# Kernel optimization log

Hardware: AMD Instinct MI355X
Metric: run time of the kernel (lower is better)

The kernel has to match this reference:

```python
import jax, jax.numpy as jnp
import numpy as np


def setup_inputs() -> dict:
    key = jax.random.key(0)
    k1, k2 = jax.random.split(key)
    B, H, W, D, K = 32, 64, 64, 64, 512
    inputs = jax.random.normal(k1, (B, H, W, D), dtype=jnp.float32)
    # codebook: (D, K) as in the keras layer (embedding_dim x num_embeddings)
    embeddings = jax.random.uniform(k2, (D, K), dtype=jnp.float32,
                                    minval=-1.0, maxval=1.0) * (3.0 / D) ** 0.5
    return {"inputs": inputs, "embeddings": embeddings}


def reference(inputs, embeddings):
    # inputs: [B, H, W, D]; embeddings: [D, K]
    D = inputs.shape[-1]
    flat = inputs.reshape(-1, D)                                   # [N, D]
    distances = (jnp.sum(flat * flat, axis=1, keepdims=True)
                 - 2.0 * (flat @ embeddings)
                 + jnp.sum(embeddings * embeddings, axis=0, keepdims=True))
    encoding_indices = jnp.argmin(distances, axis=1)               # [N]
    encoding_indices = encoding_indices.reshape(inputs.shape[:-1])  # [B, H, W]
    quantized = jnp.take(embeddings.T, encoding_indices, axis=0)   # [B, H, W, D]
    # straight-through estimator
    return inputs + jax.lax.stop_gradient(quantized - inputs)
```

## Files before the change

kernel.cpp:

```cpp
#include <hip/hip_runtime.h>


#define KC 512
#define DD 64
#define TAU 5e-4f
#define HTAU (0.5f * TAU)

typedef __attribute__((ext_vector_type(8))) short short8;
typedef __attribute__((ext_vector_type(4))) float float4v;

__device__ inline unsigned short f2bf(float f) {
    unsigned u = __float_as_uint(f);
    return (unsigned short)((u + 0x7FFF + ((u >> 16) & 1)) >> 16);
}
__device__ inline float bf2f(unsigned short b) {
    return __uint_as_float((unsigned)b << 16);
}

__global__ __launch_bounds__(256) void vq_prep(const float* __restrict__ emb,
                                               float* __restrict__ et,
                                               float* __restrict__ bias,
                                               short* __restrict__ Bh,
                                               short* __restrict__ Bl) {
    __shared__ float tile[DD][17];
    const int ct = blockIdx.x;
    const int t  = threadIdx.x;

    {
        const int d = t >> 2, c0 = (t & 3) * 4;
        float4 v = *(const float4*)(emb + (size_t)d * KC + ct * 16 + c0);
        tile[d][c0 + 0] = v.x; tile[d][c0 + 1] = v.y;
        tile[d][c0 + 2] = v.z; tile[d][c0 + 3] = v.w;
    }
    __syncthreads();

    if (t < 16) {
        float s = 0.f;
        #pragma unroll
        for (int d = 0; d < DD; ++d) { float v = tile[d][t]; s += v * v; }
        bias[ct * 16 + t] = s;
    }

    {
        const int c = t >> 4, d0 = (t & 15) * 4;
        float4 v;
        v.x = tile[d0 + 0][c]; v.y = tile[d0 + 1][c];
        v.z = tile[d0 + 2][c]; v.w = tile[d0 + 3][c];
        *(float4*)(et + (size_t)(ct * 16 + c) * DD + d0) = v;
    }

    {
        const int term = t >> 7;
        const int kc   = (t >> 6) & 1;
        const int l    = t & 63;
        const int c    = l & 15, dq = l >> 4;
        short v8[8];
        #pragma unroll
        for (int j = 0; j < 8; ++j) {
            float f = tile[kc * 32 + dq * 8 + j][c];
            unsigned short h = f2bf(f);
            v8[j] = (short)(term == 0 ? h : f2bf(f - bf2f(h)));
        }
        short* dst = (term == 0 ? Bh : Bl) + ((size_t)(ct * 2 + kc) * 64 + l) * 8;
        *(short8*)dst = *(short8*)v8;
    }
}

__global__ __launch_bounds__(512, 4) void vq_main(const float* __restrict__ x_in,
                                                  const short* __restrict__ Bh,
                                                  const short* __restrict__ Bl,
                                                  const float* __restrict__ bias,
                                                  const float* __restrict__ et,
                                                  float* __restrict__ out) {
    __shared__ __align__(16) short Bh_lds[16 * 2 * 64 * 8];
    __shared__ __align__(16) short Bl_lds[16 * 2 * 64 * 8];
    __shared__ float bias_s[KC];
    __shared__ int   k1s[8][32];
    __shared__ float gaps[8][32];

    const int t = threadIdx.x, w = t >> 6, l = t & 63;
    const int col = l & 15, quad = l >> 4;
    const int R0 = blockIdx.x * 256;
    const int wrow0 = w * 32;

    {
        const float4* srcH = (const float4*)Bh;
        const float4* srcL = (const float4*)Bl;
        float4* dstH = (float4*)Bh_lds;
        float4* dstL = (float4*)Bl_lds;
        #pragma unroll
        for (int j = 0; j < 4; ++j) {
            const int idx = t + j * 512;
            dstH[idx] = srcH[idx];
            dstL[idx] = srcL[idx];
        }
        bias_s[t] = bias[t];
    }

    short8 AH[2][2], AL[2][2];
    #pragma unroll
    for (int rt = 0; rt < 2; ++rt)
        #pragma unroll
        for (int kc = 0; kc < 2; ++kc) {
            const float* p = x_in + (size_t)(R0 + wrow0 + rt * 16 + col) * DD
                           + kc * 32 + quad * 8;
            float4 xa = *(const float4*)p;
            float4 xb = *(const float4*)(p + 4);
            float f[8] = {xa.x, xa.y, xa.z, xa.w, xb.x, xb.y, xb.z, xb.w};
            short8 hi8, lo8;
            #pragma unroll
            for (int j = 0; j < 8; ++j) {
                unsigned short h = f2bf(f[j]);
                hi8[j] = (short)h;
                lo8[j] = (short)f2bf(f[j] - bf2f(h));
            }
            AH[rt][kc] = hi8;
            AL[rt][kc] = lo8;
        }
    __syncthreads();

    float m1[2][4], m2[2][4];
    int   kb[2][4];
    #pragma unroll
    for (int rt = 0; rt < 2; ++rt)
        #pragma unroll
        for (int r = 0; r < 4; ++r) {
            m1[rt][r] = -3.4e38f; m2[rt][r] = -3.4e38f; kb[rt][r] = 0;
        }

    #pragma unroll 1
    for (int h = 0; h < 2; ++h) {
        if (h == 1) {
            __syncthreads();
            const float4* srcH = (const float4*)Bh + 2048;
            const float4* srcL = (const float4*)Bl + 2048;
            float4* dstH = (float4*)Bh_lds;
            float4* dstL = (float4*)Bl_lds;
            #pragma unroll
            for (int j = 0; j < 4; ++j) {
                const int idx = t + j * 512;
                dstH[idx] = srcH[idx];
                dstL[idx] = srcL[idx];
            }
            __syncthreads();
        }

        #pragma unroll 2
        for (int ctl = 0; ctl < 16; ++ctl) {
            short8 bh0 = *(const short8*)&Bh_lds[((ctl * 2 + 0) * 64 + l) * 8];
            short8 bh1 = *(const short8*)&Bh_lds[((ctl * 2 + 1) * 64 + l) * 8];
            short8 bl0 = *(const short8*)&Bl_lds[((ctl * 2 + 0) * 64 + l) * 8];
            short8 bl1 = *(const short8*)&Bl_lds[((ctl * 2 + 1) * 64 + l) * 8];
            const int kk = h * 256 + ctl * 16 + col;
            const float ci = -0.5f * bias_s[kk];
            #pragma unroll
            for (int rt = 0; rt < 2; ++rt) {
                float4v c = {ci, ci, ci, ci};
                c = __builtin_amdgcn_mfma_f32_16x16x32_bf16(AH[rt][0], bh0, c, 0, 0, 0);
                c = __builtin_amdgcn_mfma_f32_16x16x32_bf16(AH[rt][1], bh1, c, 0, 0, 0);
                c = __builtin_amdgcn_mfma_f32_16x16x32_bf16(AL[rt][0], bh0, c, 0, 0, 0);
                c = __builtin_amdgcn_mfma_f32_16x16x32_bf16(AL[rt][1], bh1, c, 0, 0, 0);
                c = __builtin_amdgcn_mfma_f32_16x16x32_bf16(AH[rt][0], bl0, c, 0, 0, 0);
                c = __builtin_amdgcn_mfma_f32_16x16x32_bf16(AH[rt][1], bl1, c, 0, 0, 0);
                #pragma unroll
                for (int r = 0; r < 4; ++r) {
                    float cr = c[r];
                    bool gt = cr > m1[rt][r];
                    m2[rt][r] = fmaxf(fminf(cr, m1[rt][r]), m2[rt][r]);
                    kb[rt][r] = gt ? kk : kb[rt][r];
                    m1[rt][r] = fmaxf(m1[rt][r], cr);
                }
            }
        }
    }

    #pragma unroll
    for (int rt = 0; rt < 2; ++rt)
        #pragma unroll
        for (int r = 0; r < 4; ++r) {
            float b1 = m1[rt][r], b2 = m2[rt][r];
            int   bk = kb[rt][r];
            #pragma unroll
            for (int m = 1; m <= 8; m <<= 1) {
                float o1 = __shfl_xor(b1, m, 64);
                float o2 = __shfl_xor(b2, m, 64);
                int   ok = __shfl_xor(bk, m, 64);
                float n2 = fmaxf(fmaxf(b2, o2), fminf(b1, o1));
                bool take = (o1 > b1) || (o1 == b1 && ok < bk);
                b1 = take ? o1 : b1;
                bk = take ? ok : bk;
                b2 = n2;
            }
            if (col == 0) {
                const int rowl = rt * 16 + quad * 4 + r;
                k1s[w][rowl]  = bk;
                gaps[w][rowl] = b1 - b2;
            }
        }

    {
        unsigned long long mask = __ballot((l < 32) && (gaps[w][l & 31] <= HTAU));
        mask &= 0xFFFFFFFFull;
        while (mask) {
            const int rr = __builtin_ctzll(mask);
            mask &= mask - 1;
            const size_t grow = (size_t)(R0 + wrow0 + rr) * DD;
            const int kbase = l * 8;
            float acc[8];
            #pragma unroll
            for (int j = 0; j < 8; ++j) acc[j] = 0.f;
            for (int d0 = 0; d0 < DD; d0 += 4) {
                float4 xv = *(const float4*)(x_in + grow + d0);
                #pragma unroll
                for (int j = 0; j < 8; ++j) {
                    float4 ev = *(const float4*)(et + (size_t)(kbase + j) * DD + d0);
                    acc[j] += xv.x * ev.x;
                    acc[j] += xv.y * ev.y;
                    acc[j] += xv.z * ev.z;
                    acc[j] += xv.w * ev.w;
                }
            }
            float4 b0 = *(const float4*)(bias + kbase);
            float4 b1v = *(const float4*)(bias + kbase + 4);
            float bb[8] = {b0.x, b0.y, b0.z, b0.w, b1v.x, b1v.y, b1v.z, b1v.w};
            float bv = 3.4e38f; int bk = 0;
            #pragma unroll
            for (int j = 0; j < 8; ++j) {
                float s = bb[j] - 2.f * acc[j];
                if (s < bv) { bv = s; bk = kbase + j; }
            }
            #pragma unroll
            for (int m = 1; m <= 32; m <<= 1) {
                float ov = __shfl_xor(bv, m, 64);
                int   ok = __shfl_xor(bk, m, 64);
                if (ov < bv || (ov == bv && ok < bk)) { bv = ov; bk = ok; }
            }
            if (l == 0) k1s[w][rr] = bk;
        }
    }

    {
        const int c4 = col * 4;
        #pragma unroll
        for (int i = 0; i < 8; ++i) {
            const int rowl = i * 4 + quad;
            const int bk = k1s[w][rowl];
            float4 v = *(const float4*)(et + (size_t)bk * DD + c4);
            *(float4*)(out + (size_t)(R0 + wrow0 + rowl) * DD + c4) = v;
        }
    }
}

extern "C" void kernel_launch(void* const* d_in, const int* in_sizes, int n_in,
                              void* d_out, int out_size, void* d_ws, size_t ws_size,
                              hipStream_t stream) {
    const float* x_in = (const float*)d_in[0];
    const float* emb  = (const float*)d_in[1];
    float* out = (float*)d_out;

    float* et   = (float*)d_ws;
    float* bias = et + KC * DD;
    short* Bh   = (short*)(bias + KC);
    short* Bl   = Bh + 32 * 2 * 64 * 8;

    const int N = out_size / DD;

    vq_prep<<<32, 256, 0, stream>>>(emb, et, bias, Bh, Bl);
    vq_main<<<N / 256, 512, 0, stream>>>(x_in, Bh, Bl, bias, et, out);
}
```

Baseline: 119.9 us.

## Double-buffer codebook tiles in LDS with async global-to-LDS loads

Result: no change. 119.5 us (-0.4%).

```diff
diff --git a/kernel.cpp b/kernel.cpp
--- a/kernel.cpp
+++ b/kernel.cpp
@@ -15,6 +15,12 @@
 }
 __device__ inline float bf2f(unsigned short b) {
     return __uint_as_float((unsigned)b << 16);
+}
+
+__device__ inline void gload16(const void* gsrc, void* ldst) {
+    __builtin_amdgcn_global_load_lds(
+        (const __attribute__((address_space(1))) void*)gsrc,
+        (__attribute__((address_space(3))) void*)ldst, 16, 0, 0);
 }
 
 __global__ __launch_bounds__(256) void vq_prep(const float* __restrict__ emb,
@@ -72,8 +78,8 @@
                                                   const float* __restrict__ bias,
                                                   const float* __restrict__ et,
                                                   float* __restrict__ out) {
-    __shared__ __align__(16) short Bh_lds[16 * 2 * 64 * 8];
-    __shared__ __align__(16) short Bl_lds[16 * 2 * 64 * 8];
+    __shared__ __align__(16) short Bh_lds[2][8 * 2 * 64 * 8];
+    __shared__ __align__(16) short Bl_lds[2][8 * 2 * 64 * 8];
     __shared__ float bias_s[KC];
     __shared__ int   k1s[8][32];
     __shared__ float gaps[8][32];
@@ -86,13 +92,11 @@
     {
         const float4* srcH = (const float4*)Bh;
         const float4* srcL = (const float4*)Bl;
-        float4* dstH = (float4*)Bh_lds;
-        float4* dstL = (float4*)Bl_lds;
-        #pragma unroll
-        for (int j = 0; j < 4; ++j) {
+        #pragma unroll
+        for (int j = 0; j < 2; ++j) {
             const int idx = t + j * 512;
-            dstH[idx] = srcH[idx];
-            dstL[idx] = srcL[idx];
+            gload16(srcH + idx, &Bh_lds[0][idx * 8]);
+            gload16(srcL + idx, &Bl_lds[0][idx * 8]);
         }
         bias_s[t] = bias[t];
     }
@@ -129,29 +133,31 @@
         }
 
     #pragma unroll 1
-    for (int h = 0; h < 2; ++h) {
-        if (h == 1) {
-            __syncthreads();
-            const float4* srcH = (const float4*)Bh + 2048;
-            const float4* srcL = (const float4*)Bl + 2048;
-            float4* dstH = (float4*)Bh_lds;
-            float4* dstL = (float4*)Bl_lds;
-            #pragma unroll
-            for (int j = 0; j < 4; ++j) {
+    for (int st = 0; st < 4; ++st) {
+        const int cur = st & 1;
+
+        if (st < 3) {
+            const float4* srcH = (const float4*)Bh + (st + 1) * 1024;
+            const float4* srcL = (const float4*)Bl + (st + 1) * 1024;
+            short* dH = Bh_lds[cur ^ 1];
+            short* dL = Bl_lds[cur ^ 1];
+            #pragma unroll
+            for (int j = 0; j < 2; ++j) {
                 const int idx = t + j * 512;
-                dstH[idx] = srcH[idx];
-                dstL[idx] = srcL[idx];
-            }
-            __syncthreads();
-        }
-
+                gload16(srcH + idx, dH + idx * 8);
+                gload16(srcL + idx, dL + idx * 8);
+            }
+        }
+
+        const short* BhS = Bh_lds[cur];
+        const short* BlS = Bl_lds[cur];
         #pragma unroll 2
-        for (int ctl = 0; ctl < 16; ++ctl) {
-            short8 bh0 = *(const short8*)&Bh_lds[((ctl * 2 + 0) * 64 + l) * 8];
-            short8 bh1 = *(const short8*)&Bh_lds[((ctl * 2 + 1) * 64 + l) * 8];
-            short8 bl0 = *(const short8*)&Bl_lds[((ctl * 2 + 0) * 64 + l) * 8];
-            short8 bl1 = *(const short8*)&Bl_lds[((ctl * 2 + 1) * 64 + l) * 8];
-            const int kk = h * 256 + ctl * 16 + col;
+        for (int ctl = 0; ctl < 8; ++ctl) {
+            short8 bh0 = *(const short8*)&BhS[((ctl * 2 + 0) * 64 + l) * 8];
+            short8 bh1 = *(const short8*)&BhS[((ctl * 2 + 1) * 64 + l) * 8];
+            short8 bl0 = *(const short8*)&BlS[((ctl * 2 + 0) * 64 + l) * 8];
+            short8 bl1 = *(const short8*)&BlS[((ctl * 2 + 1) * 64 + l) * 8];
+            const int kk = st * 128 + ctl * 16 + col;
             const float ci = -0.5f * bias_s[kk];
             #pragma unroll
             for (int rt = 0; rt < 2; ++rt) {
@@ -172,6 +178,8 @@
                 }
             }
         }
+
+        if (st < 3) __syncthreads();
     }
 
     #pragma unroll
```
